# Optimization experiments

Hardware: AMD Instinct MI355X
Metric: run time of the kernel (lower is better)

Reference implementation:

```python
import jax, jax.numpy as jnp
import numpy as np

REG_LAMBDA = 1e-4
NEG_SLOPE = 0.2
EPS = 1e-12


def _aggregate(edge_row, edge_col, edge_val, user_emb, item_emb, W_gcn, b_gcn, W_bi, b_bi):
    num_users = user_emb.shape[0]
    N = num_users + item_emb.shape[0]
    ego = jnp.concatenate([user_emb, item_emb], axis=0)  # [N, D]
    all_embs = [ego]
    n_layers = W_gcn.shape[0]
    for l in range(n_layers):
        # sparse adjacency spmm: side = A @ ego
        side = jax.ops.segment_sum(edge_val[:, None] * ego[edge_col], edge_row, num_segments=N)
        sum_e = side @ W_gcn[l] + b_gcn[l]
        bi_e = (ego * side) @ W_bi[l] + b_bi[l]
        ego = jax.nn.leaky_relu(sum_e + bi_e, negative_slope=NEG_SLOPE)
        # mess_dropout disabled (eval-mode); L2-normalize rows
        norm = jnp.maximum(jnp.linalg.norm(ego, axis=1, keepdims=True), EPS)
        all_embs.append(ego / norm)
    final = jnp.concatenate(all_embs, axis=1)  # [N, (L+1)*D]
    return final[:num_users], final[num_users:]


def reference(user, positive, negative, edge_row, edge_col, edge_val,
              user_emb, item_emb, W_gcn, b_gcn, W_bi, b_bi):
    users_all, items_all = _aggregate(edge_row, edge_col, edge_val,
                                      user_emb, item_emb, W_gcn, b_gcn, W_bi, b_bi)
    u = users_all[user]
    p = items_all[positive]
    n = items_all[negative]
    pos_score = jnp.sum(u * p, axis=1)
    neg_score = jnp.sum(u * n, axis=1)
    # BPR: -mean(log sigmoid(pos - neg)) == mean(softplus(neg - pos))
    bpr_loss = jnp.mean(jax.nn.softplus(neg_score - pos_score))
    ego_pos = item_emb[positive]
    ego_neg = item_emb[negative]
    B = user.shape[0]
    reg_loss = REG_LAMBDA * 0.5 * (jnp.sum(ego_pos ** 2) + jnp.sum(ego_neg ** 2)) / B
    return jnp.stack([bpr_loss, reg_loss])


def setup_inputs() -> dict:
    key = jax.random.key(0)
    ks = jax.random.split(key, 12)
    U, I, D, L, NNZ, B = 50000, 100000, 128, 3, 4800000, 4096
    N = U + I
    xav = (6.0 / (D + D)) ** 0.5
    return {
        "user": jax.random.randint(ks[0], (B,), 0, U, dtype=jnp.int32),
        "positive": jax.random.randint(ks[1], (B,), 0, I, dtype=jnp.int32),
        "negative": jax.random.randint(ks[2], (B,), 0, I, dtype=jnp.int32),
        "edge_row": jax.random.randint(ks[3], (NNZ,), 0, N, dtype=jnp.int32),
        "edge_col": jax.random.randint(ks[4], (NNZ,), 0, N, dtype=jnp.int32),
        "edge_val": jax.random.uniform(ks[5], (NNZ,), dtype=jnp.float32) / 32.0,
        "user_emb": jax.random.normal(ks[6], (U, D), dtype=jnp.float32) * 0.1,
        "item_emb": jax.random.normal(ks[7], (I, D), dtype=jnp.float32) * 0.1,
        "W_gcn": jax.random.uniform(ks[8], (L, D, D), minval=-xav, maxval=xav, dtype=jnp.float32),
        "b_gcn": jax.random.uniform(ks[9], (L, D), minval=-xav, maxval=xav, dtype=jnp.float32),
        "W_bi": jax.random.uniform(ks[10], (L, D, D), minval=-xav, maxval=xav, dtype=jnp.float32),
        "b_bi": jax.random.uniform(ks[11], (L, D), minval=-xav, maxval=xav, dtype=jnp.float32),
    }
```

## Files before the change

kernel.cpp:

```cpp
#include <hip/hip_runtime.h>
#include <math.h>

#define D 128
#define NEG_SLOPE 0.2f
#define REG_LAMBDA 1e-4f
#define NORM_EPS 1e-12f

#define RPB 256
#define RPB_SHIFT 8
#define MAXB 1024
#define CHUNK 4096
#define TCSH 14
#define KEYMAX 4096

#define XPAD 264

using bf16x8 = __attribute__((ext_vector_type(8))) short;
using f32x4  = __attribute__((ext_vector_type(4))) float;
using f32x2  = __attribute__((ext_vector_type(2))) float;

__device__ __forceinline__ float wave_red(float v){
  #pragma unroll
  for (int o = 32; o > 0; o >>= 1) v += __shfl_xor(v, o, 64);
  return v;
}

__device__ __forceinline__ unsigned short f2bf(float f){
  unsigned int u = __float_as_uint(f);
  unsigned int r = (u + 0x7fffu + ((u >> 16) & 1u)) >> 16;
  return (unsigned short)r;
}
__device__ __forceinline__ float bf_lo(unsigned int x){ return __uint_as_float(x << 16); }
__device__ __forceinline__ float bf_hi(unsigned int x){ return __uint_as_float(x & 0xffff0000u); }

__global__ __launch_bounds__(256) void toq_kernel(const float* __restrict__ src, unsigned int* __restrict__ dstb,
                                                  unsigned short* __restrict__ dst8, int npairs){
  int i = blockIdx.x*256 + threadIdx.x;
  if (i >= npairs) return;
  float2 v = ((const float2*)src)[i];
  dstb[i] = (unsigned int)f2bf(v.x) | ((unsigned int)f2bf(v.y) << 16);
  int p = __builtin_amdgcn_cvt_pk_fp8_f32(v.x, v.y, 0, false);
  dst8[i] = (unsigned short)(p & 0xffff);
}

__global__ __launch_bounds__(256) void wconv_kernel(const float* __restrict__ Wg, const float* __restrict__ Wb,
                                                    unsigned short* __restrict__ Wf, int L){
  int idx = blockIdx.x*256 + threadIdx.x;
  int total = L * 256 * D;
  if (idx >= total) return;
  int l = idx >> 15;
  int rem = idx & 32767;
  int k = rem >> 7;
  int n = rem & 127;
  float v = (k < 128) ? Wg[((size_t)l*128 + k)*D + n] : Wb[((size_t)l*128 + (k-128))*D + n];
  int ks = k >> 5, quad = (k >> 3) & 3, j = k & 7;
  int t = n >> 4, ln = (quad << 4) | (n & 15);
  Wf[(size_t)l*32768 + (((ks*8 + t)*64 + ln)*8 + j)] = f2bf(v);
}

__global__ __launch_bounds__(256) void bhist_kernel(const int* __restrict__ erow, int* __restrict__ bcnt, int nnz, int nbk){
  __shared__ int h[MAXB];
  for (int i = threadIdx.x; i < nbk; i += 256) h[i] = 0;
  __syncthreads();
  int stride = gridDim.x * 256;
  for (int e = blockIdx.x*256 + threadIdx.x; e < nnz; e += stride)
    atomicAdd(&h[erow[e] >> RPB_SHIFT], 1);
  __syncthreads();
  for (int i = threadIdx.x; i < nbk; i += 256){
    int c = h[i];
    if (c) atomicAdd(&bcnt[i], c);
  }
}

__global__ __launch_bounds__(1024) void bscan_kernel(const int* __restrict__ bcnt, int* __restrict__ bbase,
                                                     int* __restrict__ bcur, int* __restrict__ rowptr,
                                                     int nbk, int nnz, int n){
  __shared__ int tmp[1024];
  int t = threadIdx.x;
  int v = (t < nbk) ? bcnt[t] : 0;
  tmp[t] = v; __syncthreads();
  #pragma unroll
  for (int off = 1; off < 1024; off <<= 1){
    int a = (t >= off) ? tmp[t-off] : 0; __syncthreads();
    tmp[t] += a; __syncthreads();
  }
  if (t < nbk){ int b = tmp[t] - v; bbase[t] = b; bcur[t] = b; }
  if (t == 0){ bbase[nbk] = nnz; rowptr[n] = nnz; }
}

__global__ __launch_bounds__(256) void bscatter_kernel(const int* __restrict__ erow, const int* __restrict__ ecol,
                                                       const float* __restrict__ eval, int* __restrict__ bcur,
                                                       int2* __restrict__ ebuf, int nnz, int nbk){
  __shared__ int2 ls[CHUNK];
  __shared__ int gdst[CHUNK];
  __shared__ int h[MAXB];
  __shared__ int hx[MAXB];
  __shared__ int tmp[256];
  int tid = threadIdx.x;
  int base = blockIdx.x * CHUNK;
  int cn = min(CHUNK, nnz - base);
  for (int i = tid; i < nbk; i += 256) h[i] = 0;
  __syncthreads();
  for (int i = tid; i < cn; i += 256)
    atomicAdd(&h[erow[base+i] >> RPB_SHIFT], 1);
  __syncthreads();
  int b0 = tid*4;
  int c0=0,c1=0,c2=0,c3=0;
  if (b0 < nbk){
    c0 = h[b0];
    if (b0+1 < nbk) c1 = h[b0+1];
    if (b0+2 < nbk) c2 = h[b0+2];
    if (b0+3 < nbk) c3 = h[b0+3];
  }
  int tsum = c0+c1+c2+c3;
  tmp[tid] = tsum; __syncthreads();
  #pragma unroll
  for (int off = 1; off < 256; off <<= 1){
    int a = (tid >= off) ? tmp[tid-off] : 0; __syncthreads();
    tmp[tid] += a; __syncthreads();
  }
  int tbase = tmp[tid] - tsum;
  if (b0 < nbk){
    hx[b0] = tbase;
    if (b0+1 < nbk) hx[b0+1] = tbase + c0;
    if (b0+2 < nbk) hx[b0+2] = tbase + c0 + c1;
    if (b0+3 < nbk) hx[b0+3] = tbase + c0 + c1 + c2;
  }
  __syncthreads();
  for (int i = tid; i < nbk; i += 256){
    int c = h[i];
    if (c > 0){
      int gb = atomicAdd(&bcur[i], c);
      h[i] = gb - hx[i];
    }
  }
  __syncthreads();
  for (int i = tid; i < cn; i += 256){
    int r = erow[base+i];
    int b = r >> RPB_SHIFT;
    int x = ecol[base+i] | ((r & (RPB-1)) << 20);
    int lpos = atomicAdd(&hx[b], 1);
    ls[lpos] = make_int2(x, __float_as_int(eval[base+i]));
    gdst[lpos] = h[b] + lpos;
  }
  __syncthreads();
  for (int i = tid; i < cn; i += 256)
    ebuf[gdst[i]] = ls[i];
}

__global__ __launch_bounds__(256) void fscatter_kernel(const int2* __restrict__ ebuf, const int* __restrict__ bbase,
                                                       int2* __restrict__ ep, int* __restrict__ rowptr,
                                                       int Tc, int n){
  __shared__ int h[KEYMAX];
  __shared__ int tsum[256];
  int b = blockIdx.x;
  int tid = threadIdx.x;
  int s = bbase[b], e = bbase[b+1];
  int row0 = b << RPB_SHIFT;
  int nk = 256 * Tc;
  for (int i = tid; i < nk; i += 256) h[i] = 0;
  __syncthreads();
  for (int i = s + tid; i < e; i += 256){
    int x = ebuf[i].x;
    int key = ((x >> 20) & 255) * Tc + ((x & 0xFFFFF) >> TCSH);
    atomicAdd(&h[key], 1);
  }
  __syncthreads();
  int my0 = tid * Tc;
  int run = 0;
  for (int j = 0; j < Tc; j++){
    int c = h[my0 + j]; h[my0 + j] = run; run += c;
  }
  tsum[tid] = run; __syncthreads();
  #pragma unroll
  for (int off = 1; off < 256; off <<= 1){
    int a = (tid >= off) ? tsum[tid-off] : 0; __syncthreads();
    tsum[tid] += a; __syncthreads();
  }
  int bt = tsum[tid] - run;
  for (int j = 0; j < Tc; j++) h[my0 + j] += bt;
  __syncthreads();
  if (row0 + tid < n) rowptr[row0 + tid] = s + h[my0];
  __syncthreads();
  for (int i = s + tid; i < e; i += 256){
    int2 E = ebuf[i];
    int x = E.x;
    int col = x & 0xFFFFF;
    int key = ((x >> 20) & 255) * Tc + (col >> TCSH);
    int p = atomicAdd(&h[key], 1);
    ep[s + p] = make_int2(col << 7, E.y);
  }
}

__global__ __launch_bounds__(256) void spmm_kernel(const int* __restrict__ rowptr, const int2* __restrict__ ep,
                                                   const unsigned char* __restrict__ egof8,
                                                   unsigned int* __restrict__ sideb, int n){
  int w = (blockIdx.x*256 + threadIdx.x) >> 6;
  int lane = threadIdx.x & 63;
  if (w >= n) return;
  int s = rowptr[w], e = rowptr[w+1];
  int sub  = lane >> 4;
  int half = lane & 15;
  float acc[8];
  #pragma unroll
  for (int j = 0; j < 8; j++) acc[j] = 0.f;
  for (int base = s; base < e; base += 16){
    int2 E[4]; uint2 X[4];
    #pragma unroll
    for (int k = 0; k < 4; k++){
      int idx = base + 4*k + sub;
      idx = idx < e ? idx : e - 1;
      E[k] = ep[idx];
    }
    #pragma unroll
    for (int k = 0; k < 4; k++)
      X[k] = *(const uint2*)(egof8 + (size_t)(unsigned)E[k].x + half*8);
    #pragma unroll
    for (int k = 0; k < 4; k++){
      float v = (base + 4*k + sub < e) ? __int_as_float(E[k].y) : 0.f;
      f32x2 d0 = __builtin_amdgcn_cvt_pk_f32_fp8((int)X[k].x, false);
      f32x2 d1 = __builtin_amdgcn_cvt_pk_f32_fp8((int)X[k].x, true);
      f32x2 d2 = __builtin_amdgcn_cvt_pk_f32_fp8((int)X[k].y, false);
      f32x2 d3 = __builtin_amdgcn_cvt_pk_f32_fp8((int)X[k].y, true);
      acc[0] = fmaf(v, d0[0], acc[0]); acc[1] = fmaf(v, d0[1], acc[1]);
      acc[2] = fmaf(v, d1[0], acc[2]); acc[3] = fmaf(v, d1[1], acc[3]);
      acc[4] = fmaf(v, d2[0], acc[4]); acc[5] = fmaf(v, d2[1], acc[5]);
      acc[6] = fmaf(v, d3[0], acc[6]); acc[7] = fmaf(v, d3[1], acc[7]);
    }
  }
  #pragma unroll
  for (int j = 0; j < 8; j++){
    acc[j] += __shfl_xor(acc[j], 16, 64);
    acc[j] += __shfl_xor(acc[j], 32, 64);
  }
  if (lane < 16){
    unsigned int o0 = (unsigned int)f2bf(acc[0]) | ((unsigned int)f2bf(acc[1]) << 16);
    unsigned int o1 = (unsigned int)f2bf(acc[2]) | ((unsigned int)f2bf(acc[3]) << 16);
    unsigned int o2 = (unsigned int)f2bf(acc[4]) | ((unsigned int)f2bf(acc[5]) << 16);
    unsigned int o3 = (unsigned int)f2bf(acc[6]) | ((unsigned int)f2bf(acc[7]) << 16);
    *(uint4*)(sideb + (size_t)w*64 + half*4) = make_uint4(o0, o1, o2, o3);
  }
}

__global__ __launch_bounds__(256, 4) void transform_kernel(const unsigned int* __restrict__ sideb,
                                                           unsigned int* __restrict__ egob,
                                                           unsigned char* __restrict__ egof8,
                                                           const unsigned short* __restrict__ Wf,
                                                           const float* __restrict__ b1, const float* __restrict__ b2,
                                                           int n){
  __shared__ __align__(16) unsigned short X[64 * XPAD];
  int row0 = blockIdx.x * 64;
  int tid = threadIdx.x;
  for (int idx = tid; idx < 64*64; idx += 256){
    int r = idx >> 6, cp = idx & 63;
    int row = row0 + r;
    unsigned int sv = 0, pv = 0;
    if (row < n){
      unsigned int s2 = sideb[(size_t)row*64 + cp];
      unsigned int eb = egob[(size_t)row*64 + cp];
      sv = s2;
      pv = (unsigned int)f2bf(bf_lo(s2) * bf_lo(eb)) | ((unsigned int)f2bf(bf_hi(s2) * bf_hi(eb)) << 16);
    }
    *(unsigned int*)&X[r*XPAD + 2*cp]       = sv;
    *(unsigned int*)&X[r*XPAD + 128 + 2*cp] = pv;
  }
  __syncthreads();

  int wave = tid >> 6, lane = tid & 63;
  int wr0 = wave * 16;
  int m = lane & 15, quad = lane >> 4;

  f32x4 acc[8];
  #pragma unroll
  for (int t = 0; t < 8; t++) acc[t] = (f32x4){0.f, 0.f, 0.f, 0.f};

  const unsigned short* arow = &X[(wr0 + m)*XPAD + quad*8];
  #pragma unroll
  for (int ks = 0; ks < 8; ks++){
    bf16x8 a = *(const bf16x8*)(arow + ks*32);
    #pragma unroll
    for (int t = 0; t < 8; t++){
      bf16x8 b = *(const bf16x8*)&Wf[((ks*8 + t)*64 + lane)*8];
      acc[t] = __builtin_amdgcn_mfma_f32_16x16x32_bf16(a, b, acc[t], 0, 0, 0);
    }
  }

  unsigned short* ego16 = (unsigned short*)egob;
  #pragma unroll
  for (int t = 0; t < 8; t++){
    int col = t*16 + m;
    float bb = b1[col] + b2[col];
    #pragma unroll
    for (int r = 0; r < 4; r++){
      int row = row0 + wr0 + quad*4 + r;
      if (row < n){
        float v = acc[t][r] + bb;
        v = v > 0.f ? v : NEG_SLOPE*v;
        ego16[(size_t)row*D + col] = f2bf(v);
        egof8[(size_t)row*D + col] =
            (unsigned char)(__builtin_amdgcn_cvt_pk_fp8_f32(v, v, 0, false) & 0xff);
      }
    }
  }
}

__global__ __launch_bounds__(256) void score_kernel(const unsigned int* __restrict__ egob, const int* __restrict__ user,
                                                    const int* __restrict__ pos, const int* __restrict__ neg,
                                                    float* __restrict__ pacc, float* __restrict__ nacc,
                                                    int B, int U, int normalize){
  int w = (blockIdx.x*256 + threadIdx.x) >> 6;
  int lane = threadIdx.x & 63;
  if (w >= B) return;
  size_t ur = (size_t)user[w] * 64;
  size_t pr = ((size_t)U + pos[w]) * 64;
  size_t nr = ((size_t)U + neg[w]) * 64;
  unsigned int ub = egob[ur + lane], pb = egob[pr + lane], nb = egob[nr + lane];
  float ux = bf_lo(ub), uy = bf_hi(ub);
  float px = bf_lo(pb), py = bf_hi(pb);
  float nx = bf_lo(nb), ny = bf_hi(nb);
  float dup = ux*px + uy*py;
  float dun = ux*nx + uy*ny;
  float nu  = ux*ux + uy*uy;
  float np  = px*px + py*py;
  float nn  = nx*nx + ny*ny;
  dup = wave_red(dup); dun = wave_red(dun);
  nu = wave_red(nu); np = wave_red(np); nn = wave_red(nn);
  if (lane == 0){
    if (normalize){
      float inu = 1.f / fmaxf(sqrtf(nu), NORM_EPS);
      float inp = 1.f / fmaxf(sqrtf(np), NORM_EPS);
      float inn = 1.f / fmaxf(sqrtf(nn), NORM_EPS);
      pacc[w] += dup * inu * inp;
      nacc[w] += dun * inu * inn;
    } else {
      pacc[w] += dup;
      nacc[w] += dun;
    }
  }
}

__global__ __launch_bounds__(256) void reg_kernel(const float* __restrict__ item, const int* __restrict__ pos,
                                                  const int* __restrict__ neg, float* __restrict__ reg_out, int B){
  int w = (blockIdx.x*256 + threadIdx.x) >> 6;
  int lane = threadIdx.x & 63;
  if (w >= B) return;
  const float2* it = (const float2*)item;
  float2 pv = it[(size_t)pos[w]*64 + lane];
  float2 nv = it[(size_t)neg[w]*64 + lane];
  float v = pv.x*pv.x + pv.y*pv.y + nv.x*nv.x + nv.y*nv.y;
  v = wave_red(v);
  if (lane == 0) atomicAdd(reg_out, v);
}

__global__ __launch_bounds__(256) void final_kernel(const float* __restrict__ pacc, const float* __restrict__ nacc,
                                                    const float* __restrict__ reg_sum, float* __restrict__ out, int B){
  __shared__ float red[256];
  float s = 0.f;
  for (int i = threadIdx.x; i < B; i += 256){
    float x = nacc[i] - pacc[i];
    s += (x > 0.f) ? x + log1pf(expf(-x)) : log1pf(expf(x));
  }
  red[threadIdx.x] = s; __syncthreads();
  for (int o = 128; o > 0; o >>= 1){
    if (threadIdx.x < o) red[threadIdx.x] += red[threadIdx.x + o];
    __syncthreads();
  }
  if (threadIdx.x == 0){
    out[0] = red[0] / (float)B;
    out[1] = REG_LAMBDA * 0.5f * reg_sum[0] / (float)B;
  }
}

extern "C" void kernel_launch(void* const* d_in, const int* in_sizes, int n_in,
                              void* d_out, int out_size, void* d_ws, size_t ws_size,
                              hipStream_t stream) {
  const int*   user = (const int*)d_in[0];
  const int*   pos  = (const int*)d_in[1];
  const int*   neg  = (const int*)d_in[2];
  const int*   erow = (const int*)d_in[3];
  const int*   ecol = (const int*)d_in[4];
  const float* eval = (const float*)d_in[5];
  const float* uemb = (const float*)d_in[6];
  const float* iemb = (const float*)d_in[7];
  const float* Wg   = (const float*)d_in[8];
  const float* bg   = (const float*)d_in[9];
  const float* Wb   = (const float*)d_in[10];
  const float* bb   = (const float*)d_in[11];

  int B   = in_sizes[0];
  int NNZ = in_sizes[3];
  int U   = in_sizes[6] / D;
  int I   = in_sizes[7] / D;
  int N   = U + I;
  int L   = in_sizes[9] / D;
  int nbk = (N + RPB - 1) >> RPB_SHIFT;
  int Tc  = (N + (1 << TCSH) - 1) >> TCSH;

  char* wsp = (char*)d_ws;
  auto alloc = [&](size_t bytes) -> char* {
    char* p = wsp; wsp += (bytes + 255) & ~(size_t)255; return p;
  };
  size_t side_bytes = (size_t)N * D * 2;
  size_t ebuf_bytes = (size_t)NNZ * 8;
  unsigned int*  sideb  = (unsigned int*)alloc(side_bytes > ebuf_bytes ? side_bytes : ebuf_bytes);
  unsigned int*  egob   = (unsigned int*)alloc((size_t)N * D * 2);
  unsigned short* egof8 = (unsigned short*)alloc((size_t)N * D);
  int2*          ep     = (int2*) alloc((size_t)NNZ * 8);
  unsigned short* Wf    = (unsigned short*)alloc((size_t)L * 256 * D * 2);
  int*           rowptr = (int*)  alloc((size_t)(N + 1) * 4);
  int*           bcnt   = (int*)  alloc((size_t)MAXB * 4);
  int*           bbase  = (int*)  alloc((size_t)(MAXB + 1) * 4);
  int*           bcur   = (int*)  alloc((size_t)MAXB * 4);
  float*         pacc   = (float*)alloc((size_t)B * 4);
  float*         nacc   = (float*)alloc((size_t)B * 4);
  float*         regs   = (float*)alloc(256);
  int2*          ebuf   = (int2*)sideb;

  hipMemsetAsync(bcnt, 0, (size_t)nbk * 4, stream);
  hipMemsetAsync(pacc, 0, (size_t)B * 4, stream);
  hipMemsetAsync(nacc, 0, (size_t)B * 4, stream);
  hipMemsetAsync(regs, 0, 4, stream);

  toq_kernel<<<(U*64 + 255) / 256, 256, 0, stream>>>(uemb, egob, egof8, U*64);
  toq_kernel<<<(I*64 + 255) / 256, 256, 0, stream>>>(iemb, egob + (size_t)U*64, egof8 + (size_t)U*64, I*64);
  wconv_kernel<<<(L*256*D + 255) / 256, 256, 0, stream>>>(Wg, Wb, Wf, L);

  bhist_kernel<<<2048, 256, 0, stream>>>(erow, bcnt, NNZ, nbk);
  bscan_kernel<<<1, 1024, 0, stream>>>(bcnt, bbase, bcur, rowptr, nbk, NNZ, N);
  bscatter_kernel<<<(NNZ + CHUNK - 1) / CHUNK, 256, 0, stream>>>(erow, ecol, eval, bcur, ebuf, NNZ, nbk);
  fscatter_kernel<<<nbk, 256, 0, stream>>>(ebuf, bbase, ep, rowptr, Tc, N);

  score_kernel<<<(B + 3) / 4, 256, 0, stream>>>(egob, user, pos, neg, pacc, nacc, B, U, 0);

  for (int l = 0; l < L; l++){
    spmm_kernel<<<(N + 3) / 4, 256, 0, stream>>>(rowptr, ep, (const unsigned char*)egof8, sideb, N);
    transform_kernel<<<(N + 63) / 64, 256, 0, stream>>>(
        sideb, egob, (unsigned char*)egof8, Wf + (size_t)l * 256 * D,
        bg + (size_t)l * D, bb + (size_t)l * D, N);
    score_kernel<<<(B + 3) / 4, 256, 0, stream>>>(egob, user, pos, neg, pacc, nacc, B, U, 1);
  }

  reg_kernel<<<(B + 3) / 4, 256, 0, stream>>>(iemb, pos, neg, regs, B);
  final_kernel<<<1, 256, 0, stream>>>(pacc, nacc, regs, (float*)d_out, B);
}
```

Measured before the change: 911.5 us.

## Fuse SpMM gather with dense transform into one per-layer kernel, ping-pong buffers

```diff
diff --git a/kernel.cpp b/kernel.cpp
--- a/kernel.cpp
+++ b/kernel.cpp
@@ -9,7 +9,7 @@
 #define RPB 256
 #define RPB_SHIFT 8
 #define MAXB 1024
-#define CHUNK 4096
+#define CHUNK 8192
 #define TCSH 14
 #define KEYMAX 4096
 
@@ -88,46 +88,33 @@
   if (t == 0){ bbase[nbk] = nnz; rowptr[n] = nnz; }
 }
 
-__global__ __launch_bounds__(256) void bscatter_kernel(const int* __restrict__ erow, const int* __restrict__ ecol,
-                                                       const float* __restrict__ eval, int* __restrict__ bcur,
-                                                       int2* __restrict__ ebuf, int nnz, int nbk){
+__global__ __launch_bounds__(1024) void bscatter_kernel(const int* __restrict__ erow, const int* __restrict__ ecol,
+                                                        const float* __restrict__ eval, int* __restrict__ bcur,
+                                                        int2* __restrict__ ebuf, int nnz, int nbk){
   __shared__ int2 ls[CHUNK];
-  __shared__ int gdst[CHUNK];
+  __shared__ unsigned short bkt[CHUNK];
   __shared__ int h[MAXB];
   __shared__ int hx[MAXB];
-  __shared__ int tmp[256];
+  __shared__ int tmp[1024];
   int tid = threadIdx.x;
   int base = blockIdx.x * CHUNK;
   int cn = min(CHUNK, nnz - base);
-  for (int i = tid; i < nbk; i += 256) h[i] = 0;
-  __syncthreads();
-  for (int i = tid; i < cn; i += 256)
+  for (int i = tid; i < nbk; i += 1024) h[i] = 0;
+  __syncthreads();
+  for (int i = tid; i < cn; i += 1024)
     atomicAdd(&h[erow[base+i] >> RPB_SHIFT], 1);
   __syncthreads();
-  int b0 = tid*4;
-  int c0=0,c1=0,c2=0,c3=0;
-  if (b0 < nbk){
-    c0 = h[b0];
-    if (b0+1 < nbk) c1 = h[b0+1];
-    if (b0+2 < nbk) c2 = h[b0+2];
-    if (b0+3 < nbk) c3 = h[b0+3];
-  }
-  int tsum = c0+c1+c2+c3;
-  tmp[tid] = tsum; __syncthreads();
-  #pragma unroll
-  for (int off = 1; off < 256; off <<= 1){
+  int v = (tid < nbk) ? h[tid] : 0;
+  tmp[tid] = v; __syncthreads();
+  #pragma unroll
+  for (int off = 1; off < 1024; off <<= 1){
     int a = (tid >= off) ? tmp[tid-off] : 0; __syncthreads();
     tmp[tid] += a; __syncthreads();
   }
-  int tbase = tmp[tid] - tsum;
-  if (b0 < nbk){
-    hx[b0] = tbase;
-    if (b0+1 < nbk) hx[b0+1] = tbase + c0;
-    if (b0+2 < nbk) hx[b0+2] = tbase + c0 + c1;
-    if (b0+3 < nbk) hx[b0+3] = tbase + c0 + c1 + c2;
-  }
-  __syncthreads();
-  for (int i = tid; i < nbk; i += 256){
+  int excl = tmp[tid] - v;
+  if (tid < nbk) hx[tid] = excl;
+  __syncthreads();
+  for (int i = tid; i < nbk; i += 1024){
     int c = h[i];
     if (c > 0){
       int gb = atomicAdd(&bcur[i], c);
@@ -135,17 +122,17 @@
     }
   }
   __syncthreads();
-  for (int i = tid; i < cn; i += 256){
+  for (int i = tid; i < cn; i += 1024){
     int r = erow[base+i];
     int b = r >> RPB_SHIFT;
     int x = ecol[base+i] | ((r & (RPB-1)) << 20);
     int lpos = atomicAdd(&hx[b], 1);
     ls[lpos] = make_int2(x, __float_as_int(eval[base+i]));
-    gdst[lpos] = h[b] + lpos;
-  }
-  __syncthreads();
-  for (int i = tid; i < cn; i += 256)
-    ebuf[gdst[i]] = ls[i];
+    bkt[lpos] = (unsigned short)b;
+  }
+  __syncthreads();
+  for (int i = tid; i < cn; i += 1024)
+    ebuf[h[bkt[i]] + i] = ls[i];
 }
 
 __global__ __launch_bounds__(256) void fscatter_kernel(const int2* __restrict__ ebuf, const int* __restrict__ bbase,
@@ -192,87 +179,83 @@
   }
 }
 
-__global__ __launch_bounds__(256) void spmm_kernel(const int* __restrict__ rowptr, const int2* __restrict__ ep,
-                                                   const unsigned char* __restrict__ egof8,
-                                                   unsigned int* __restrict__ sideb, int n){
-  int w = (blockIdx.x*256 + threadIdx.x) >> 6;
-  int lane = threadIdx.x & 63;
-  if (w >= n) return;
-  int s = rowptr[w], e = rowptr[w+1];
+__global__ __launch_bounds__(256, 4) void layer_kernel(const int* __restrict__ rowptr, const int2* __restrict__ ep,
+                                                       const unsigned char* __restrict__ egof8_in,
+                                                       const unsigned int* __restrict__ egob_in,
+                                                       unsigned int* __restrict__ egob_out,
+                                                       unsigned char* __restrict__ egof8_out,
+                                                       const unsigned short* __restrict__ Wf,
+                                                       const float* __restrict__ b1, const float* __restrict__ b2,
+                                                       int n){
+  __shared__ __align__(16) unsigned short X[64 * XPAD];
+  int row0 = blockIdx.x * 64;
+  int tid = threadIdx.x, wave = tid >> 6, lane = tid & 63;
   int sub  = lane >> 4;
   int half = lane & 15;
-  float acc[8];
-  #pragma unroll
-  for (int j = 0; j < 8; j++) acc[j] = 0.f;
-  for (int base = s; base < e; base += 16){
-    int2 E[4]; uint2 X[4];
+
+  for (int r = 0; r < 16; r++){
+    int lr  = wave*16 + r;
+    int row = row0 + lr;
+    float acc[8];
     #pragma unroll
-    for (int k = 0; k < 4; k++){
-      int idx = base + 4*k + sub;
-      idx = idx < e ? idx : e - 1;
-      E[k] = ep[idx];
-    }
-    #pragma unroll
-    for (int k = 0; k < 4; k++)
-      X[k] = *(const uint2*)(egof8 + (size_t)(unsigned)E[k].x + half*8);
-    #pragma unroll
-    for (int k = 0; k < 4; k++){
-      float v = (base + 4*k + sub < e) ? __int_as_float(E[k].y) : 0.f;
-      f32x2 d0 = __builtin_amdgcn_cvt_pk_f32_fp8((int)X[k].x, false);
-      f32x2 d1 = __builtin_amdgcn_cvt_pk_f32_fp8((int)X[k].x, true);
-      f32x2 d2 = __builtin_amdgcn_cvt_pk_f32_fp8((int)X[k].y, false);
-      f32x2 d3 = __builtin_amdgcn_cvt_pk_f32_fp8((int)X[k].y, true);
-      acc[0] = fmaf(v, d0[0], acc[0]); acc[1] = fmaf(v, d0[1], acc[1]);
-      acc[2] = fmaf(v, d1[0], acc[2]); acc[3] = fmaf(v, d1[1], acc[3]);
-      acc[4] = fmaf(v, d2[0], acc[4]); acc[5] = fmaf(v, d2[1], acc[5]);
-      acc[6] = fmaf(v, d3[0], acc[6]); acc[7] = fmaf(v, d3[1], acc[7]);
-    }
-  }
-  #pragma unroll
-  for (int j = 0; j < 8; j++){
-    acc[j] += __shfl_xor(acc[j], 16, 64);
-    acc[j] += __shfl_xor(acc[j], 32, 64);
-  }
-  if (lane < 16){
-    unsigned int o0 = (unsigned int)f2bf(acc[0]) | ((unsigned int)f2bf(acc[1]) << 16);
-    unsigned int o1 = (unsigned int)f2bf(acc[2]) | ((unsigned int)f2bf(acc[3]) << 16);
-    unsigned int o2 = (unsigned int)f2bf(acc[4]) | ((unsigned int)f2bf(acc[5]) << 16);
-    unsigned int o3 = (unsigned int)f2bf(acc[6]) | ((unsigned int)f2bf(acc[7]) << 16);
-    *(uint4*)(sideb + (size_t)w*64 + half*4) = make_uint4(o0, o1, o2, o3);
-  }
-}
-
-__global__ __launch_bounds__(256, 4) void transform_kernel(const unsigned int* __restrict__ sideb,
-                                                           unsigned int* __restrict__ egob,
-                                                           unsigned char* __restrict__ egof8,
-                                                           const unsigned short* __restrict__ Wf,
-                                                           const float* __restrict__ b1, const float* __restrict__ b2,
-                                                           int n){
-  __shared__ __align__(16) unsigned short X[64 * XPAD];
-  int row0 = blockIdx.x * 64;
-  int tid = threadIdx.x;
-  for (int idx = tid; idx < 64*64; idx += 256){
-    int r = idx >> 6, cp = idx & 63;
-    int row = row0 + r;
-    unsigned int sv = 0, pv = 0;
+    for (int j = 0; j < 8; j++) acc[j] = 0.f;
     if (row < n){
-      unsigned int s2 = sideb[(size_t)row*64 + cp];
-      unsigned int eb = egob[(size_t)row*64 + cp];
-      sv = s2;
-      pv = (unsigned int)f2bf(bf_lo(s2) * bf_lo(eb)) | ((unsigned int)f2bf(bf_hi(s2) * bf_hi(eb)) << 16);
-    }
-    *(unsigned int*)&X[r*XPAD + 2*cp]       = sv;
-    *(unsigned int*)&X[r*XPAD + 128 + 2*cp] = pv;
-  }
-  __syncthreads();
-
-  int wave = tid >> 6, lane = tid & 63;
+      int s = rowptr[row], e = rowptr[row+1];
+      for (int base = s; base < e; base += 16){
+        int2 E[4]; uint2 Xg[4];
+        #pragma unroll
+        for (int k = 0; k < 4; k++){
+          int idx = base + 4*k + sub;
+          idx = idx < e ? idx : e - 1;
+          E[k] = ep[idx];
+        }
+        #pragma unroll
+        for (int k = 0; k < 4; k++)
+          Xg[k] = *(const uint2*)(egof8_in + (size_t)(unsigned)E[k].x + half*8);
+        #pragma unroll
+        for (int k = 0; k < 4; k++){
+          float v = (base + 4*k + sub < e) ? __int_as_float(E[k].y) : 0.f;
+          f32x2 d0 = __builtin_amdgcn_cvt_pk_f32_fp8((int)Xg[k].x, false);
+          f32x2 d1 = __builtin_amdgcn_cvt_pk_f32_fp8((int)Xg[k].x, true);
+          f32x2 d2 = __builtin_amdgcn_cvt_pk_f32_fp8((int)Xg[k].y, false);
+          f32x2 d3 = __builtin_amdgcn_cvt_pk_f32_fp8((int)Xg[k].y, true);
+          acc[0] = fmaf(v, d0[0], acc[0]); acc[1] = fmaf(v, d0[1], acc[1]);
+          acc[2] = fmaf(v, d1[0], acc[2]); acc[3] = fmaf(v, d1[1], acc[3]);
+          acc[4] = fmaf(v, d2[0], acc[4]); acc[5] = fmaf(v, d2[1], acc[5]);
+          acc[6] = fmaf(v, d3[0], acc[6]); acc[7] = fmaf(v, d3[1], acc[7]);
+        }
+      }
+      #pragma unroll
+      for (int j = 0; j < 8; j++){
+        acc[j] += __shfl_xor(acc[j], 16, 64);
+        acc[j] += __shfl_xor(acc[j], 32, 64);
+      }
+    }
+    if (lane < 16){
+      uint4 sv = make_uint4(0,0,0,0), pv = make_uint4(0,0,0,0);
+      if (row < n){
+        uint4 eg = *(const uint4*)(egob_in + (size_t)row*64 + half*4);
+        sv.x = (unsigned int)f2bf(acc[0]) | ((unsigned int)f2bf(acc[1]) << 16);
+        sv.y = (unsigned int)f2bf(acc[2]) | ((unsigned int)f2bf(acc[3]) << 16);
+        sv.z = (unsigned int)f2bf(acc[4]) | ((unsigned int)f2bf(acc[5]) << 16);
+        sv.w = (unsigned int)f2bf(acc[6]) | ((unsigned int)f2bf(acc[7]) << 16);
+        pv.x = (unsigned int)f2bf(acc[0]*bf_lo(eg.x)) | ((unsigned int)f2bf(acc[1]*bf_hi(eg.x)) << 16);
+        pv.y = (unsigned int)f2bf(acc[2]*bf_lo(eg.y)) | ((unsigned int)f2bf(acc[3]*bf_hi(eg.y)) << 16);
+        pv.z = (unsigned int)f2bf(acc[4]*bf_lo(eg.z)) | ((unsigned int)f2bf(acc[5]*bf_hi(eg.z)) << 16);
+        pv.w = (unsigned int)f2bf(acc[6]*bf_lo(eg.w)) | ((unsigned int)f2bf(acc[7]*bf_hi(eg.w)) << 16);
+      }
+      *(uint4*)&X[lr*XPAD + half*8]       = sv;
+      *(uint4*)&X[lr*XPAD + 128 + half*8] = pv;
+    }
+  }
+  __syncthreads();
+
   int wr0 = wave * 16;
   int m = lane & 15, quad = lane >> 4;
 
-  f32x4 acc[8];
-  #pragma unroll
-  for (int t = 0; t < 8; t++) acc[t] = (f32x4){0.f, 0.f, 0.f, 0.f};
+  f32x4 acc2[8];
+  #pragma unroll
+  for (int t = 0; t < 8; t++) acc2[t] = (f32x4){0.f, 0.f, 0.f, 0.f};
 
   const unsigned short* arow = &X[(wr0 + m)*XPAD + quad*8];
   #pragma unroll
@@ -281,11 +264,11 @@
     #pragma unroll
     for (int t = 0; t < 8; t++){
       bf16x8 b = *(const bf16x8*)&Wf[((ks*8 + t)*64 + lane)*8];
-      acc[t] = __builtin_amdgcn_mfma_f32_16x16x32_bf16(a, b, acc[t], 0, 0, 0);
-    }
-  }
-
-  unsigned short* ego16 = (unsigned short*)egob;
+      acc2[t] = __builtin_amdgcn_mfma_f32_16x16x32_bf16(a, b, acc2[t], 0, 0, 0);
+    }
+  }
+
+  unsigned short* ego16 = (unsigned short*)egob_out;
   #pragma unroll
   for (int t = 0; t < 8; t++){
     int col = t*16 + m;
@@ -294,10 +277,10 @@
     for (int r = 0; r < 4; r++){
       int row = row0 + wr0 + quad*4 + r;
       if (row < n){
-        float v = acc[t][r] + bb;
+        float v = acc2[t][r] + bb;
         v = v > 0.f ? v : NEG_SLOPE*v;
         ego16[(size_t)row*D + col] = f2bf(v);
-        egof8[(size_t)row*D + col] =
+        egof8_out[(size_t)row*D + col] =
             (unsigned char)(__builtin_amdgcn_cvt_pk_fp8_f32(v, v, 0, false) & 0xff);
       }
     }
@@ -400,11 +383,11 @@
   auto alloc = [&](size_t bytes) -> char* {
     char* p = wsp; wsp += (bytes + 255) & ~(size_t)255; return p;
   };
-  size_t side_bytes = (size_t)N * D * 2;
-  size_t ebuf_bytes = (size_t)NNZ * 8;
-  unsigned int*  sideb  = (unsigned int*)alloc(side_bytes > ebuf_bytes ? side_bytes : ebuf_bytes);
-  unsigned int*  egob   = (unsigned int*)alloc((size_t)N * D * 2);
-  unsigned short* egof8 = (unsigned short*)alloc((size_t)N * D);
+  unsigned int*  egob0  = (unsigned int*)alloc((size_t)N * D * 2);
+  unsigned int*  egob1  = (unsigned int*)alloc((size_t)N * D * 2);
+  unsigned short* egof80 = (unsigned short*)alloc((size_t)N * D);
+  unsigned short* egof81 = (unsigned short*)alloc((size_t)N * D);
+  int2*          ebuf   = (int2*) alloc((size_t)NNZ * 8);
   int2*          ep     = (int2*) alloc((size_t)NNZ * 8);
   unsigned short* Wf    = (unsigned short*)alloc((size_t)L * 256 * D * 2);
   int*           rowptr = (int*)  alloc((size_t)(N + 1) * 4);
@@ -414,30 +397,35 @@
   float*         pacc   = (float*)alloc((size_t)B * 4);
   float*         nacc   = (float*)alloc((size_t)B * 4);
   float*         regs   = (float*)alloc(256);
-  int2*          ebuf   = (int2*)sideb;
+
+  unsigned int*   egob[2]  = {egob0, egob1};
+  unsigned short* egof8[2] = {egof80, egof81};
 
   hipMemsetAsync(bcnt, 0, (size_t)nbk * 4, stream);
   hipMemsetAsync(pacc, 0, (size_t)B * 4, stream);
   hipMemsetAsync(nacc, 0, (size_t)B * 4, stream);
   hipMemsetAsync(regs, 0, 4, stream);
 
-  toq_kernel<<<(U*64 + 255) / 256, 256, 0, stream>>>(uemb, egob, egof8, U*64);
-  toq_kernel<<<(I*64 + 255) / 256, 256, 0, stream>>>(iemb, egob + (size_t)U*64, egof8 + (size_t)U*64, I*64);
+  toq_kernel<<<(U*64 + 255) / 256, 256, 0, stream>>>(uemb, egob0, egof80, U*64);
+  toq_kernel<<<(I*64 + 255) / 256, 256, 0, stream>>>(iemb, egob0 + (size_t)U*64, egof80 + (size_t)U*64, I*64);
   wconv_kernel<<<(L*256*D + 255) / 256, 256, 0, stream>>>(Wg, Wb, Wf, L);
 
-  bhist_kernel<<<2048, 256, 0, stream>>>(erow, bcnt, NNZ, nbk);
+  bhist_kernel<<<512, 256, 0, stream>>>(erow, bcnt, NNZ, nbk);
   bscan_kernel<<<1, 1024, 0, stream>>>(bcnt, bbase, bcur, rowptr, nbk, NNZ, N);
-  bscatter_kernel<<<(NNZ + CHUNK - 1) / CHUNK, 256, 0, stream>>>(erow, ecol, eval, bcur, ebuf, NNZ, nbk);
+  bscatter_kernel<<<(NNZ + CHUNK - 1) / CHUNK, 1024, 0, stream>>>(erow, ecol, eval, bcur, ebuf, NNZ, nbk);
   fscatter_kernel<<<nbk, 256, 0, stream>>>(ebuf, bbase, ep, rowptr, Tc, N);
 
-  score_kernel<<<(B + 3) / 4, 256, 0, stream>>>(egob, user, pos, neg, pacc, nacc, B, U, 0);
+  score_kernel<<<(B + 3) / 4, 256, 0, stream>>>(egob0, user, pos, neg, pacc, nacc, B, U, 0);
 
   for (int l = 0; l < L; l++){
-    spmm_kernel<<<(N + 3) / 4, 256, 0, stream>>>(rowptr, ep, (const unsigned char*)egof8, sideb, N);
-    transform_kernel<<<(N + 63) / 64, 256, 0, stream>>>(
-        sideb, egob, (unsigned char*)egof8, Wf + (size_t)l * 256 * D,
+    int cur = l & 1, nxt = cur ^ 1;
+    layer_kernel<<<(N + 63) / 64, 256, 0, stream>>>(
+        rowptr, ep,
+        (const unsigned char*)egof8[cur], egob[cur],
+        egob[nxt], (unsigned char*)egof8[nxt],
+        Wf + (size_t)l * 256 * D,
         bg + (size_t)l * D, bb + (size_t)l * D, N);
-    score_kernel<<<(B + 3) / 4, 256, 0, stream>>>(egob, user, pos, neg, pacc, nacc, B, U, 1);
+    score_kernel<<<(B + 3) / 4, 256, 0, stream>>>(egob[nxt], user, pos, neg, pacc, nacc, B, U, 1);
   }
 
   reg_kernel<<<(B + 3) / 4, 256, 0, stream>>>(iemb, pos, neg, regs, B);
```

Result: slower. 974.0 us (+6.9%).
